# Kernel tuning notes

Hardware: AMD Instinct MI355X
Metric: run time of the kernel (lower is better)

The kernel has to match this reference:

```python
import jax, jax.numpy as jnp
import numpy as np

SELECTED_NUM = 4096
BN_EPS = 1e-5


def _conv1d(x, w, pad):
    # x: [B, C_in, L], w: [C_out, C_in, K]
    return jax.lax.conv_general_dilated(
        x, w, window_strides=(1,), padding=[(pad, pad)],
        dimension_numbers=('NCH', 'OIH', 'NCH'))


def _bn(x, g, b, m, v):
    # eval-mode BatchNorm1d over channel dim of [B, C, L]
    inv = g / jnp.sqrt(v + BN_EPS)
    return x * inv[None, :, None] + (b - m * inv)[None, :, None]


def setup_inputs() -> dict:
    key = jax.random.key(0)
    ks = jax.random.split(key, 16)
    B, N, CODE, NCLS = 4, 262144, 7, 3
    inp = {
        'box_preds': jax.random.normal(ks[0], (B, N, CODE), jnp.float32),
        'cls_preds': jax.random.normal(ks[1], (B, N, NCLS), jnp.float32),
        # conv_share: Conv1d(10,32,3) + BN(32) + ReLU + Conv1d(32,64,3) + BN(64) + ReLU
        'conv1_w': jax.random.normal(ks[2], (32, 10, 3), jnp.float32) * 0.1,
        'bn1_g': jax.random.uniform(ks[3], (32,), jnp.float32, 0.5, 1.5),
        'bn1_b': jax.random.normal(ks[4], (32,), jnp.float32) * 0.1,
        'bn1_m': jax.random.normal(ks[5], (32,), jnp.float32) * 0.1,
        'bn1_v': jax.random.uniform(ks[6], (32,), jnp.float32, 0.5, 1.5),
        'conv2_w': jax.random.normal(ks[7], (64, 32, 3), jnp.float32) * 0.1,
        'bn2_g': jax.random.uniform(ks[8], (64,), jnp.float32, 0.5, 1.5),
        'bn2_b': jax.random.normal(ks[9], (64,), jnp.float32) * 0.1,
        'bn2_m': jax.random.normal(ks[10], (64,), jnp.float32) * 0.1,
        'bn2_v': jax.random.uniform(ks[11], (64,), jnp.float32, 0.5, 1.5),
        # heads: Conv1d(64,5,1,bias=True), Conv1d(64,1,1,bias=True)
        'bin_w': jax.random.normal(ks[12], (5, 64, 1), jnp.float32) * 0.1,
        'bin_b': jnp.full((5,), -float(np.log((1 - 0.01) / 0.01)), jnp.float32),
        'res_w': jax.random.normal(ks[13], (1, 64, 1), jnp.float32) * 0.001,
        'res_b': jnp.zeros((1,), jnp.float32),
    }
    return inp


def reference(box_preds, cls_preds, conv1_w, bn1_g, bn1_b, bn1_m, bn1_v,
              conv2_w, bn2_g, bn2_b, bn2_m, bn2_v, bin_w, bin_b, res_w, res_b):
    # ---- proposal_layer: per-batch sigmoid(max-cls-score) topk + gather ----
    score = jax.nn.sigmoid(jnp.max(cls_preds, axis=-1))          # [B, N]
    _, sel = jax.lax.top_k(score, SELECTED_NUM)                  # [B, K]
    box_sel = jnp.take_along_axis(box_preds, sel[:, :, None], axis=1)  # [B, K, 7]
    cls_sel = jnp.take_along_axis(cls_preds, sel[:, :, None], axis=1)  # [B, K, 3]

    # ---- conv_share + heads over channel-first layout [B, 10, K] ----
    x = jnp.concatenate([box_sel, cls_sel], axis=-1).transpose(0, 2, 1)  # [B, 10, K]
    x = jax.nn.relu(_bn(_conv1d(x, conv1_w, 1), bn1_g, bn1_b, bn1_m, bn1_v))
    x = jax.nn.relu(_bn(_conv1d(x, conv2_w, 1), bn2_g, bn2_b, bn2_m, bn2_v))  # [B, 64, K]

    iou_bin = _conv1d(x, bin_w, 0) + bin_b[None, :, None]        # [B, 5, K]
    iou_res = _conv1d(x, res_w, 0) + res_b[None, :, None]        # [B, 1, K]

    iou_preds_bin = iou_bin.transpose(0, 2, 1)                   # [B, K, 5]
    iou_preds_residual = iou_res.transpose(0, 2, 1)              # [B, K, 1]
    return iou_preds_bin, iou_preds_residual, box_sel, cls_sel
```

## Files before the change

### kernel.cpp

```cpp
#include <hip/hip_runtime.h>
#include <stdint.h>

#define NPTS 262144
#define NB 4
#define KSEL 4096
#define CAP 8192
#define SLICE_LEN 1024
#define CBLK 128
#define HBLK 64

#define OFF_BITS  0ULL
#define OFF_H8P   (4ULL*NPTS*NB)
#define OFF_H12   (OFF_H8P + 4ULL*256*HBLK*NB)
#define OFF_CTRL  (OFF_H12 + 4ULL*4096*NB)
#define OFF_GRANK (OFF_CTRL + 1024ULL)
#define OFF_CAND  (OFF_GRANK + 4ULL*CAP*NB)
#define WS_NEEDED (OFF_CAND + 8ULL*CAP*NB)

#define OBIN 0
#define ORES (NB*KSEL*5)
#define OBOX (ORES + NB*KSEL)
#define OCLS (OBOX + NB*KSEL*7)


__device__ __forceinline__ uint32_t key_of(float mx) {
    uint32_t b = __float_as_uint(mx);
    uint32_t mask = ((int32_t)b >> 31) | 0x80000000u;
    return b ^ mask;
}

__device__ __forceinline__ void suffix_scan_256(volatile uint32_t* part, int tid) {
    #pragma unroll
    for (int off = 1; off < 256; off <<= 1) {
        uint32_t v = part[tid] + ((tid + off < 256) ? part[tid + off] : 0u);
        __syncthreads();
        part[tid] = v;
        __syncthreads();
    }
}

__global__ __launch_bounds__(256) void k_score_hist(
    const float* __restrict__ cls, uint32_t* __restrict__ bits, uint32_t* __restrict__ h8p,
    uint32_t* __restrict__ h12, uint32_t* __restrict__ grank, uint32_t* __restrict__ ctrl)
{
    __shared__ uint32_t lh[8][256];
    for (int i = threadIdx.x; i < 2048; i += 256) ((uint32_t*)lh)[i] = 0;
    __syncthreads();
    int b = blockIdx.y, bx = blockIdx.x;
    int sub = threadIdx.x >> 5;
    for (int it = 0; it < 4; ++it) {
        int chunk = bx * 1024 + it * 256 + threadIdx.x;
        const float4* p = (const float4*)(cls + ((size_t)b * NPTS + (size_t)chunk * 4) * 3);
        float4 v0 = p[0], v1 = p[1], v2 = p[2];
        uint4 o;
        o.x = key_of(fmaxf(fmaxf(v0.x, v0.y), v0.z));
        o.y = key_of(fmaxf(fmaxf(v0.w, v1.x), v1.y));
        o.z = key_of(fmaxf(fmaxf(v1.z, v1.w), v2.x));
        o.w = key_of(fmaxf(fmaxf(v2.y, v2.z), v2.w));
        ((uint4*)(bits + (size_t)b * NPTS))[chunk] = o;
        atomicAdd(&lh[sub][o.x >> 24], 1u);
        atomicAdd(&lh[sub][o.y >> 24], 1u);
        atomicAdd(&lh[sub][o.z >> 24], 1u);
        atomicAdd(&lh[sub][o.w >> 24], 1u);
    }
    if (bx == 1) {
        uint4* z = (uint4*)(h12 + (size_t)b * 4096);
        #pragma unroll
        for (int i = 0; i < 4; ++i) z[threadIdx.x + i * 256] = make_uint4(0u, 0u, 0u, 0u);
    } else if (bx == 2) {
        uint4* zg = (uint4*)(grank + (size_t)b * CAP);
        #pragma unroll
        for (int i = 0; i < 8; ++i) zg[threadIdx.x + i * 256] = make_uint4(0u, 0u, 0u, 0u);
    } else if (bx == 3 && threadIdx.x == 0) {
        ctrl[b * 16 + 3] = 0u;
    }
    __syncthreads();
    uint32_t c = 0;
    #pragma unroll
    for (int s = 0; s < 8; ++s) c += lh[s][threadIdx.x];
    h8p[((size_t)b * HBLK + bx) * 256 + threadIdx.x] = c;
}

__global__ __launch_bounds__(256) void k_hist12(
    const uint32_t* __restrict__ bits, const uint32_t* __restrict__ h8p,
    uint32_t* __restrict__ ctrl, uint32_t* __restrict__ h12)
{
    __shared__ uint32_t lh[4096];
    __shared__ uint32_t part[257];
    __shared__ uint32_t P8s;
    int b = blockIdx.y, bx = blockIdx.x;
    int tid = threadIdx.x;
    for (int i = tid; i < 4096; i += 256) lh[i] = 0;
    uint32_t sum = 0;
    const uint32_t* hp = h8p + (size_t)b * HBLK * 256 + tid;
    #pragma unroll 8
    for (int blk = 0; blk < HBLK; ++blk) sum += hp[blk * 256];
    part[tid] = sum;
    if (tid == 0) part[256] = 0u;
    __syncthreads();
    suffix_scan_256(part, tid);
    {
        uint32_t si = part[tid], sn = part[tid + 1];
        if (si >= (uint32_t)KSEL && sn < (uint32_t)KSEL) {
            P8s = (uint32_t)tid;
            if (bx == 0) { ctrl[b * 16 + 0] = (uint32_t)tid; ctrl[b * 16 + 1] = sn; }
        }
    }
    __syncthreads();
    const uint32_t P8 = P8s;
    for (int it = 0; it < 4; ++it) {
        int chunk = bx * 1024 + it * 256 + tid;
        uint4 v = ((const uint4*)(bits + (size_t)b * NPTS))[chunk];
        if ((v.x >> 24) == P8) atomicAdd(&lh[(v.x >> 12) & 0xFFFu], 1u);
        if ((v.y >> 24) == P8) atomicAdd(&lh[(v.y >> 12) & 0xFFFu], 1u);
        if ((v.z >> 24) == P8) atomicAdd(&lh[(v.z >> 12) & 0xFFFu], 1u);
        if ((v.w >> 24) == P8) atomicAdd(&lh[(v.w >> 12) & 0xFFFu], 1u);
    }
    __syncthreads();
    for (int i = tid; i < 4096; i += 256) {
        uint32_t c = lh[i];
        if (c) atomicAdd(&h12[(size_t)b * 4096 + i], c);
    }
}

__global__ __launch_bounds__(256) void k_compact(
    const uint32_t* __restrict__ bits, const uint32_t* __restrict__ h12,
    uint32_t* __restrict__ ctrl, uint64_t* __restrict__ cand)
{
    __shared__ uint32_t bins[4096];
    __shared__ uint32_t part[257];
    __shared__ uint32_t segS, Ts;
    __shared__ uint32_t wbase[4];
    int b = blockIdx.y, bx = blockIdx.x;
    int tid = threadIdx.x;
    const uint4* src = (const uint4*)(h12 + (size_t)b * 4096);
    for (int i = tid; i < 1024; i += 256) ((uint4*)bins)[i] = src[i];
    __syncthreads();
    {
        uint32_t s = 0;
        int base2 = tid * 16;
        #pragma unroll
        for (int j = 0; j < 16; ++j) s += bins[base2 + j];
        part[tid] = s;
        if (tid == 0) part[256] = 0u;
    }
    __syncthreads();
    const uint32_t K = (uint32_t)KSEL - ctrl[b * 16 + 1];
    suffix_scan_256(part, tid);
    {
        uint32_t si = part[tid], sn = part[tid + 1];
        if (si >= K && sn < K) segS = (uint32_t)tid;
    }
    __syncthreads();
    if (tid < 16) {
        uint32_t seg = segS;
        uint32_t above = part[seg + 1];
        uint32_t cnt = above;
        for (int j = 15; j >= tid; --j) cnt += bins[seg * 16 + j];
        uint32_t cntn = cnt - bins[seg * 16 + tid];
        if (cnt >= K && cntn < K) {
            Ts = (ctrl[b * 16 + 0] << 12) | (seg * 16 + (uint32_t)tid);
        }
    }
    __syncthreads();
    const uint32_t T = Ts;
    const int lane = tid & 63, wave = tid >> 6;
    const uint64_t lmask = (1ull << lane) - 1ull;

    int chunk0 = bx * 512 + tid;
    const uint4* sb = (const uint4*)(bits + (size_t)b * NPTS);
    uint4 v0 = sb[chunk0];
    uint4 v1 = sb[chunk0 + 256];
    uint32_t ks[8] = {v0.x, v0.y, v0.z, v0.w, v1.x, v1.y, v1.z, v1.w};
    bool sel[8];
    #pragma unroll
    for (int i = 0; i < 8; ++i) sel[i] = (ks[i] >> 12) >= T;

    uint32_t wsum = 0;
    #pragma unroll
    for (int i = 0; i < 8; ++i) wsum += (uint32_t)__popcll(__ballot(sel[i]));
    if (lane == 0) wbase[wave] = wsum;
    __syncthreads();
    if (tid == 0) {
        uint32_t c0 = wbase[0], c1 = wbase[1], c2 = wbase[2], c3 = wbase[3];
        uint32_t tot = c0 + c1 + c2 + c3;
        uint32_t base = tot ? atomicAdd(&ctrl[b * 16 + 3], tot) : 0u;
        wbase[0] = base;
        wbase[1] = base + c0;
        wbase[2] = base + c0 + c1;
        wbase[3] = base + c0 + c1 + c2;
    }
    __syncthreads();
    uint32_t off = wbase[wave];
    #pragma unroll
    for (int i = 0; i < 8; ++i) {
        uint64_t m = __ballot(sel[i]);
        if (sel[i]) {
            uint32_t pos = off + (uint32_t)__popcll(m & lmask);
            uint32_t n = (uint32_t)(chunk0 + (i < 4 ? 0 : 256)) * 4 + (uint32_t)(i & 3);
            if (pos < CAP)
                cand[(size_t)b * CAP + pos] = ((uint64_t)(~ks[i]) << 32) | (uint64_t)n;
        }
        off += (uint32_t)__popcll(m);
    }
}

__global__ __launch_bounds__(256) void k_rank1(
    const uint64_t* __restrict__ cand, const uint32_t* __restrict__ ctrl,
    uint32_t* __restrict__ grank)
{
    __shared__ uint64_t keys[SLICE_LEN];
    int b = blockIdx.z;
    uint32_t C = ctrl[b * 16 + 3];
    if (C > CAP) C = CAP;
    uint32_t ig0 = blockIdx.x * 1024;
    uint32_t sk0 = blockIdx.y * SLICE_LEN;
    if (ig0 >= C || sk0 >= C) return;
    uint32_t nk = C - sk0; if (nk > SLICE_LEN) nk = SLICE_LEN;
    const uint64_t* cb = cand + (size_t)b * CAP;
    for (uint32_t i = threadIdx.x; i < nk; i += 256) keys[i] = cb[sk0 + i];
    __syncthreads();
    uint64_t me[4];
    uint32_t idx[4], r[4] = {0u, 0u, 0u, 0u};
    #pragma unroll
    for (int q = 0; q < 4; ++q) {
        idx[q] = ig0 + (uint32_t)q * 256 + threadIdx.x;
        me[q] = (idx[q] < C) ? cb[idx[q]] : ~0ull;
    }
    #pragma unroll 8
    for (uint32_t i = 0; i < nk; ++i) {
        uint64_t k = keys[i];
        r[0] += (k < me[0]) ? 1u : 0u;
        r[1] += (k < me[1]) ? 1u : 0u;
        r[2] += (k < me[2]) ? 1u : 0u;
        r[3] += (k < me[3]) ? 1u : 0u;
    }
    #pragma unroll
    for (int q = 0; q < 4; ++q)
        if (idx[q] < C) atomicAdd(&grank[b * CAP + idx[q]], r[q]);
}

__global__ __launch_bounds__(256) void k_rank2(
    const uint64_t* __restrict__ cand, const uint32_t* __restrict__ ctrl,
    const uint32_t* __restrict__ grank,
    const float* __restrict__ box, const float* __restrict__ cls, float* __restrict__ out)
{
    int b = blockIdx.y;
    uint32_t C = ctrl[b * 16 + 3];
    if (C > CAP) C = CAP;
    uint32_t item = blockIdx.x * 256 + threadIdx.x;
    if (blockIdx.x * 256 >= C) return;
    if (item >= C) return;
    uint64_t me = cand[(size_t)b * CAP + item];
    uint32_t rank = grank[b * CAP + item];
    if (rank < KSEL) {
        uint32_t n = (uint32_t)me;
        const float* bp = box + ((size_t)b * NPTS + n) * 7;
        float* ob = out + OBOX + ((size_t)b * KSEL + rank) * 7;
        #pragma unroll
        for (int c = 0; c < 7; ++c) ob[c] = bp[c];
        const float* cp = cls + ((size_t)b * NPTS + n) * 3;
        float* oc = out + OCLS + ((size_t)b * KSEL + rank) * 3;
        #pragma unroll
        for (int c = 0; c < 3; ++c) oc[c] = cp[c];
    }
}

__global__ __launch_bounds__(256) void k_conv(
    const float* __restrict__ c1w, const float* __restrict__ g1v, const float* __restrict__ b1v,
    const float* __restrict__ m1v, const float* __restrict__ v1v,
    const float* __restrict__ c2w, const float* __restrict__ g2v, const float* __restrict__ b2v,
    const float* __restrict__ m2v, const float* __restrict__ v2v,
    const float* __restrict__ binw, const float* __restrict__ binb,
    const float* __restrict__ resw, const float* __restrict__ resb,
    float* __restrict__ out)
{
    __shared__ __align__(16) float w1s[960];
    __shared__ __align__(16) float b1s[32];
    __shared__ __align__(16) float w2s[6144];
    __shared__ __align__(16) float b2s[64];
    __shared__ __align__(16) float hws[6][64];
    __shared__ __align__(16) float xin[10][80];
    __shared__ __align__(16) float x1s[32][68];
    __shared__ __align__(16) float x2t[64][68];

    int tid = threadIdx.x;
    int b = blockIdx.y;
    int tile0 = blockIdx.x * 64;
    const float* boxsel = out + OBOX + (size_t)b * KSEL * 7;
    const float* clssel = out + OCLS + (size_t)b * KSEL * 3;

    for (int t = tid; t < 960; t += 256) {
        int c = t / 30, r = t - c * 30, i = r / 3, tap = r - i * 3;
        float inv = g1v[c] * rsqrtf(v1v[c] + 1e-5f);
        w1s[(i * 3 + tap) * 32 + c] = c1w[t] * inv;
    }
    if (tid < 32) {
        float inv = g1v[tid] * rsqrtf(v1v[tid] + 1e-5f);
        b1s[tid] = b1v[tid] - m1v[tid] * inv;
    }
    for (int t = tid; t < 6144; t += 256) {
        int o = t / 96, r = t - o * 96, i = r / 3, tap = r - i * 3;
        float inv = g2v[o] * rsqrtf(v2v[o] + 1e-5f);
        w2s[(i * 3 + tap) * 64 + o] = c2w[t] * inv;
    }
    if (tid >= 64 && tid < 128) {
        int o = tid - 64;
        float inv = g2v[o] * rsqrtf(v2v[o] + 1e-5f);
        b2s[o] = b2v[o] - m2v[o] * inv;
    }
    for (int t = tid; t < 384; t += 256)
        ((float*)hws)[t] = (t < 320) ? binw[t] : resw[t - 320];

    for (int u = tid; u < 680; u += 256) {
        int c = u / 68, k2 = u - c * 68;
        int g = tile0 + k2 - 2;
        float val = 0.f;
        if (g >= 0 && g < KSEL) val = (c < 7) ? boxsel[g * 7 + c] : clssel[g * 3 + (c - 7)];
        xin[c][k2] = val;
    }
    __syncthreads();

    {
        int c = tid & 31, kg = tid >> 5;
        int k0 = kg * 9;
        int nk = 66 - k0; if (nk > 9) nk = 9;
        float a[9];
        #pragma unroll
        for (int kk = 0; kk < 9; ++kk) a[kk] = b1s[c];
        #pragma unroll 2
        for (int i = 0; i < 10; ++i) {
            float xv[11];
            #pragma unroll
            for (int j = 0; j < 11; ++j) xv[j] = xin[i][k0 + j];
            #pragma unroll
            for (int tap = 0; tap < 3; ++tap) {
                float w = w1s[(i * 3 + tap) * 32 + c];
                #pragma unroll
                for (int kk = 0; kk < 9; ++kk) a[kk] = fmaf(w, xv[kk + tap], a[kk]);
            }
        }
        for (int kk = 0; kk < nk; ++kk) {
            int k = k0 + kk, gp = tile0 + k - 1;
            x1s[c][k] = (gp >= 0 && gp < KSEL) ? fmaxf(a[kk], 0.f) : 0.f;
        }
    }
    __syncthreads();

    {
        int o = tid & 63, pg = tid >> 6;
        int p0 = pg * 16;
        float acc[16];
        float bz = b2s[o];
        #pragma unroll
        for (int kk = 0; kk < 16; ++kk) acc[kk] = bz;
        #pragma unroll 4
        for (int i = 0; i < 32; ++i) {
            float4 xq[5];
            const float4* xr = (const float4*)&x1s[i][p0];
            #pragma unroll
            for (int q = 0; q < 5; ++q) xq[q] = xr[q];
            const float* xf = (const float*)xq;
            float w0 = w2s[(i * 3 + 0) * 64 + o];
            float w1 = w2s[(i * 3 + 1) * 64 + o];
            float w2 = w2s[(i * 3 + 2) * 64 + o];
            #pragma unroll
            for (int kk = 0; kk < 16; ++kk) {
                float t0 = fmaf(w0, xf[kk], acc[kk]);
                t0 = fmaf(w1, xf[kk + 1], t0);
                acc[kk] = fmaf(w2, xf[kk + 2], t0);
            }
        }
        #pragma unroll
        for (int kk = 0; kk < 16; ++kk)
            x2t[p0 + kk][o] = fmaxf(acc[kk], 0.f);
    }
    __syncthreads();

    {
        int p = tid & 63, g = tid >> 6;
        const float4* xr = (const float4*)&x2t[p][0];
        const float4* hw4 = (const float4*)hws;
        size_t gpos = (size_t)b * KSEL + (size_t)(tile0 + p);
        if (g < 2) {
            int j0 = g * 2, j1 = j0 + 1;
            float s0 = 0.f, s1 = 0.f;
            #pragma unroll
            for (int q = 0; q < 16; ++q) {
                float4 xv = xr[q];
                float4 wa = hw4[j0 * 16 + q];
                float4 wb = hw4[j1 * 16 + q];
                s0 = fmaf(xv.x, wa.x, s0); s0 = fmaf(xv.y, wa.y, s0);
                s0 = fmaf(xv.z, wa.z, s0); s0 = fmaf(xv.w, wa.w, s0);
                s1 = fmaf(xv.x, wb.x, s1); s1 = fmaf(xv.y, wb.y, s1);
                s1 = fmaf(xv.z, wb.z, s1); s1 = fmaf(xv.w, wb.w, s1);
            }
            out[OBIN + gpos * 5 + j0] = s0 + binb[j0];
            out[OBIN + gpos * 5 + j1] = s1 + binb[j1];
        } else {
            int j = (g == 2) ? 4 : 5;
            float s = 0.f;
            #pragma unroll
            for (int q = 0; q < 16; ++q) {
                float4 xv = xr[q];
                float4 wa = hw4[j * 16 + q];
                s = fmaf(xv.x, wa.x, s); s = fmaf(xv.y, wa.y, s);
                s = fmaf(xv.z, wa.z, s); s = fmaf(xv.w, wa.w, s);
            }
            if (g == 2) out[OBIN + gpos * 5 + 4] = s + binb[4];
            else        out[ORES + gpos]         = s + resb[0];
        }
    }
}

extern "C" void kernel_launch(void* const* d_in, const int* in_sizes, int n_in,
                              void* d_out, int out_size, void* d_ws, size_t ws_size,
                              hipStream_t stream)
{
    const float* box  = (const float*)d_in[0];
    const float* cls  = (const float*)d_in[1];
    const float* c1w  = (const float*)d_in[2];
    const float* g1   = (const float*)d_in[3];
    const float* b1   = (const float*)d_in[4];
    const float* m1   = (const float*)d_in[5];
    const float* v1   = (const float*)d_in[6];
    const float* c2w  = (const float*)d_in[7];
    const float* g2   = (const float*)d_in[8];
    const float* b2   = (const float*)d_in[9];
    const float* m2   = (const float*)d_in[10];
    const float* v2   = (const float*)d_in[11];
    const float* binw = (const float*)d_in[12];
    const float* binb = (const float*)d_in[13];
    const float* resw = (const float*)d_in[14];
    const float* resb = (const float*)d_in[15];
    float* out = (float*)d_out;
    char* ws = (char*)d_ws;
    if (ws_size < WS_NEEDED) return;

    uint32_t* bits  = (uint32_t*)(ws + OFF_BITS);
    uint32_t* h8p   = (uint32_t*)(ws + OFF_H8P);
    uint32_t* h12   = (uint32_t*)(ws + OFF_H12);
    uint32_t* ctrl  = (uint32_t*)(ws + OFF_CTRL);
    uint32_t* grank = (uint32_t*)(ws + OFF_GRANK);
    uint64_t* cand  = (uint64_t*)(ws + OFF_CAND);

    k_score_hist<<<dim3(HBLK, NB), 256, 0, stream>>>(cls, bits, h8p, h12, grank, ctrl);
    k_hist12<<<dim3(HBLK, NB), 256, 0, stream>>>(bits, h8p, ctrl, h12);
    k_compact<<<dim3(CBLK, NB), 256, 0, stream>>>(bits, h12, ctrl, cand);
    k_rank1<<<dim3(CAP / 1024, CAP / 1024, NB), 256, 0, stream>>>(cand, ctrl, grank);
    k_rank2<<<dim3(CAP / 256, NB), 256, 0, stream>>>(cand, ctrl, grank, box, cls, out);
    k_conv<<<dim3(64, NB), 256, 0, stream>>>(c1w, g1, b1, m1, v1, c2w, g2, b2, m2, v2,
                                             binw, binb, resw, resb, out);
}
```

Measured before the change: 75.63 us.

## Replace two-pass radix select with single 16-bit histogram and last-block threshold

The 8-bit then 12-bit histogram passes are replaced by one 16-bit key histogram built while the keys are computed. A fixed window of bins near the expected top scores is counted in shared memory, and everything else goes straight to global atomics. The last block to finish, detected with an atomic counter, scans the histogram and writes the threshold, so the second pass over the keys and the threshold search in k_compact both go away. The cost is coarser threshold bins, hence more candidates, and possible global-atomic contention when scores fall outside the window.

```diff
diff --git a/kernel.cpp b/kernel.cpp
--- a/kernel.cpp
+++ b/kernel.cpp
@@ -6,13 +6,13 @@
 #define KSEL 4096
 #define CAP 8192
 #define SLICE_LEN 1024
-#define CBLK 128
-#define HBLK 64
+#define KBLK 256
+#define WIN_LO 0xB800u
+#define WIN_N  0x1000u
 
 #define OFF_BITS  0ULL
-#define OFF_H8P   (4ULL*NPTS*NB)
-#define OFF_H12   (OFF_H8P + 4ULL*256*HBLK*NB)
-#define OFF_CTRL  (OFF_H12 + 4ULL*4096*NB)
+#define OFF_H16   (4ULL*NPTS*NB)
+#define OFF_CTRL  (OFF_H16 + 4ULL*65536*NB)
 #define OFF_GRANK (OFF_CTRL + 1024ULL)
 #define OFF_CAND  (OFF_GRANK + 4ULL*CAP*NB)
 #define WS_NEEDED (OFF_CAND + 8ULL*CAP*NB)
@@ -39,152 +39,121 @@
     }
 }
 
-__global__ __launch_bounds__(256) void k_score_hist(
-    const float* __restrict__ cls, uint32_t* __restrict__ bits, uint32_t* __restrict__ h8p,
-    uint32_t* __restrict__ h12, uint32_t* __restrict__ grank, uint32_t* __restrict__ ctrl)
-{
-    __shared__ uint32_t lh[8][256];
-    for (int i = threadIdx.x; i < 2048; i += 256) ((uint32_t*)lh)[i] = 0;
-    __syncthreads();
-    int b = blockIdx.y, bx = blockIdx.x;
-    int sub = threadIdx.x >> 5;
-    for (int it = 0; it < 4; ++it) {
-        int chunk = bx * 1024 + it * 256 + threadIdx.x;
-        const float4* p = (const float4*)(cls + ((size_t)b * NPTS + (size_t)chunk * 4) * 3);
-        float4 v0 = p[0], v1 = p[1], v2 = p[2];
-        uint4 o;
-        o.x = key_of(fmaxf(fmaxf(v0.x, v0.y), v0.z));
-        o.y = key_of(fmaxf(fmaxf(v0.w, v1.x), v1.y));
-        o.z = key_of(fmaxf(fmaxf(v1.z, v1.w), v2.x));
-        o.w = key_of(fmaxf(fmaxf(v2.y, v2.z), v2.w));
-        ((uint4*)(bits + (size_t)b * NPTS))[chunk] = o;
-        atomicAdd(&lh[sub][o.x >> 24], 1u);
-        atomicAdd(&lh[sub][o.y >> 24], 1u);
-        atomicAdd(&lh[sub][o.z >> 24], 1u);
-        atomicAdd(&lh[sub][o.w >> 24], 1u);
-    }
-    if (bx == 1) {
-        uint4* z = (uint4*)(h12 + (size_t)b * 4096);
-        #pragma unroll
-        for (int i = 0; i < 4; ++i) z[threadIdx.x + i * 256] = make_uint4(0u, 0u, 0u, 0u);
-    } else if (bx == 2) {
-        uint4* zg = (uint4*)(grank + (size_t)b * CAP);
-        #pragma unroll
-        for (int i = 0; i < 8; ++i) zg[threadIdx.x + i * 256] = make_uint4(0u, 0u, 0u, 0u);
-    } else if (bx == 3 && threadIdx.x == 0) {
-        ctrl[b * 16 + 3] = 0u;
-    }
-    __syncthreads();
-    uint32_t c = 0;
-    #pragma unroll
-    for (int s = 0; s < 8; ++s) c += lh[s][threadIdx.x];
-    h8p[((size_t)b * HBLK + bx) * 256 + threadIdx.x] = c;
-}
-
-__global__ __launch_bounds__(256) void k_hist12(
-    const uint32_t* __restrict__ bits, const uint32_t* __restrict__ h8p,
-    uint32_t* __restrict__ ctrl, uint32_t* __restrict__ h12)
-{
-    __shared__ uint32_t lh[4096];
+__global__ __launch_bounds__(256) void k_init(
+    uint4* __restrict__ h16v, uint4* __restrict__ grankv, uint32_t* __restrict__ ctrl)
+{
+    int bx = blockIdx.x, tid = threadIdx.x;
+    uint4 z = make_uint4(0u, 0u, 0u, 0u);
+    if (bx < 32) {
+        int i = bx * 2048 + tid;
+        #pragma unroll
+        for (int k = 0; k < 8; ++k) h16v[i + k * 256] = z;
+    } else {
+        int i = (bx - 32) * 1024 + tid;
+        #pragma unroll
+        for (int k = 0; k < 4; ++k) grankv[i + k * 256] = z;
+        if (bx == 32 && tid < 64) ctrl[tid] = 0u;
+    }
+}
+
+__global__ __launch_bounds__(256) void k_keys(
+    const float* __restrict__ cls, uint32_t* __restrict__ bits,
+    uint32_t* __restrict__ h16, uint32_t* __restrict__ ctrl)
+{
+    __shared__ uint32_t lh[WIN_N];
     __shared__ uint32_t part[257];
-    __shared__ uint32_t P8s;
-    int b = blockIdx.y, bx = blockIdx.x;
-    int tid = threadIdx.x;
-    for (int i = tid; i < 4096; i += 256) lh[i] = 0;
-    uint32_t sum = 0;
-    const uint32_t* hp = h8p + (size_t)b * HBLK * 256 + tid;
-    #pragma unroll 8
-    for (int blk = 0; blk < HBLK; ++blk) sum += hp[blk * 256];
-    part[tid] = sum;
+    __shared__ uint32_t segS, aboveS;
+    __shared__ int amLastS;
+    int b = blockIdx.y, bx = blockIdx.x, tid = threadIdx.x;
+    for (int i = tid; i < (int)WIN_N; i += 256) lh[i] = 0;
+    __syncthreads();
+
+    int chunk = bx * 256 + tid;
+    const float4* p = (const float4*)(cls + ((size_t)b * NPTS + (size_t)chunk * 4) * 3);
+    float4 v0 = p[0], v1 = p[1], v2 = p[2];
+    uint4 o;
+    o.x = key_of(fmaxf(fmaxf(v0.x, v0.y), v0.z));
+    o.y = key_of(fmaxf(fmaxf(v0.w, v1.x), v1.y));
+    o.z = key_of(fmaxf(fmaxf(v1.z, v1.w), v2.x));
+    o.w = key_of(fmaxf(fmaxf(v2.y, v2.z), v2.w));
+    ((uint4*)(bits + (size_t)b * NPTS))[chunk] = o;
+    uint32_t ks[4] = {o.x, o.y, o.z, o.w};
+    uint32_t* h16b = h16 + (size_t)b * 65536;
+    #pragma unroll
+    for (int i = 0; i < 4; ++i) {
+        uint32_t hi = ks[i] >> 16;
+        uint32_t d = hi - WIN_LO;
+        if (d < WIN_N) atomicAdd(&lh[d], 1u);
+        else           atomicAdd(&h16b[hi], 1u);
+    }
+    __syncthreads();
+    for (int i = tid; i < (int)WIN_N; i += 256) {
+        uint32_t c = lh[i];
+        if (c) atomicAdd(&h16b[WIN_LO + i], c);
+    }
+    __syncthreads();
+    __threadfence();
+    if (tid == 0) {
+        uint32_t r = atomicAdd(&ctrl[b * 16 + 15], 1u);
+        amLastS = (r == (uint32_t)(KBLK - 1));
+    }
+    __syncthreads();
+    if (!amLastS) return;
+
+    const uint4* h4 = (const uint4*)h16b;
+    uint32_t s = 0;
+    #pragma unroll 16
+    for (int q = 0; q < 64; ++q) {
+        uint4 v = h4[tid * 64 + q];
+        s += v.x + v.y + v.z + v.w;
+    }
+    part[tid] = s;
+    if (tid == 0) part[256] = 0u;
+    __syncthreads();
+    suffix_scan_256(part, tid);
+    if (part[tid] >= (uint32_t)KSEL && part[tid + 1] < (uint32_t)KSEL) segS = (uint32_t)tid;
+    __syncthreads();
+    if (tid == 0) aboveS = part[segS + 1];
+    __syncthreads();
+    uint32_t binv = h16b[segS * 256 + tid];
+    __syncthreads();
+    part[tid] = binv;
     if (tid == 0) part[256] = 0u;
     __syncthreads();
     suffix_scan_256(part, tid);
     {
-        uint32_t si = part[tid], sn = part[tid + 1];
-        if (si >= (uint32_t)KSEL && sn < (uint32_t)KSEL) {
-            P8s = (uint32_t)tid;
-            if (bx == 0) { ctrl[b * 16 + 0] = (uint32_t)tid; ctrl[b * 16 + 1] = sn; }
-        }
-    }
-    __syncthreads();
-    const uint32_t P8 = P8s;
-    for (int it = 0; it < 4; ++it) {
-        int chunk = bx * 1024 + it * 256 + tid;
-        uint4 v = ((const uint4*)(bits + (size_t)b * NPTS))[chunk];
-        if ((v.x >> 24) == P8) atomicAdd(&lh[(v.x >> 12) & 0xFFFu], 1u);
-        if ((v.y >> 24) == P8) atomicAdd(&lh[(v.y >> 12) & 0xFFFu], 1u);
-        if ((v.z >> 24) == P8) atomicAdd(&lh[(v.z >> 12) & 0xFFFu], 1u);
-        if ((v.w >> 24) == P8) atomicAdd(&lh[(v.w >> 12) & 0xFFFu], 1u);
-    }
-    __syncthreads();
-    for (int i = tid; i < 4096; i += 256) {
-        uint32_t c = lh[i];
-        if (c) atomicAdd(&h12[(size_t)b * 4096 + i], c);
+        uint32_t above = aboveS;
+        if (above + part[tid] >= (uint32_t)KSEL && above + part[tid + 1] < (uint32_t)KSEL)
+            ctrl[b * 16 + 2] = segS * 256 + (uint32_t)tid;
     }
 }
 
 __global__ __launch_bounds__(256) void k_compact(
-    const uint32_t* __restrict__ bits, const uint32_t* __restrict__ h12,
-    uint32_t* __restrict__ ctrl, uint64_t* __restrict__ cand)
-{
-    __shared__ uint32_t bins[4096];
-    __shared__ uint32_t part[257];
-    __shared__ uint32_t segS, Ts;
+    const uint32_t* __restrict__ bits, const uint32_t* __restrict__ ctrl,
+    uint64_t* __restrict__ cand)
+{
     __shared__ uint32_t wbase[4];
-    int b = blockIdx.y, bx = blockIdx.x;
-    int tid = threadIdx.x;
-    const uint4* src = (const uint4*)(h12 + (size_t)b * 4096);
-    for (int i = tid; i < 1024; i += 256) ((uint4*)bins)[i] = src[i];
-    __syncthreads();
-    {
-        uint32_t s = 0;
-        int base2 = tid * 16;
-        #pragma unroll
-        for (int j = 0; j < 16; ++j) s += bins[base2 + j];
-        part[tid] = s;
-        if (tid == 0) part[256] = 0u;
-    }
-    __syncthreads();
-    const uint32_t K = (uint32_t)KSEL - ctrl[b * 16 + 1];
-    suffix_scan_256(part, tid);
-    {
-        uint32_t si = part[tid], sn = part[tid + 1];
-        if (si >= K && sn < K) segS = (uint32_t)tid;
-    }
-    __syncthreads();
-    if (tid < 16) {
-        uint32_t seg = segS;
-        uint32_t above = part[seg + 1];
-        uint32_t cnt = above;
-        for (int j = 15; j >= tid; --j) cnt += bins[seg * 16 + j];
-        uint32_t cntn = cnt - bins[seg * 16 + tid];
-        if (cnt >= K && cntn < K) {
-            Ts = (ctrl[b * 16 + 0] << 12) | (seg * 16 + (uint32_t)tid);
-        }
-    }
-    __syncthreads();
-    const uint32_t T = Ts;
+    int b = blockIdx.y, tid = threadIdx.x;
+    uint32_t T = ctrl[b * 16 + 2];
     const int lane = tid & 63, wave = tid >> 6;
     const uint64_t lmask = (1ull << lane) - 1ull;
 
-    int chunk0 = bx * 512 + tid;
-    const uint4* sb = (const uint4*)(bits + (size_t)b * NPTS);
-    uint4 v0 = sb[chunk0];
-    uint4 v1 = sb[chunk0 + 256];
-    uint32_t ks[8] = {v0.x, v0.y, v0.z, v0.w, v1.x, v1.y, v1.z, v1.w};
-    bool sel[8];
-    #pragma unroll
-    for (int i = 0; i < 8; ++i) sel[i] = (ks[i] >> 12) >= T;
+    int chunk = blockIdx.x * 256 + tid;
+    uint4 v = ((const uint4*)(bits + (size_t)b * NPTS))[chunk];
+    uint32_t ks[4] = {v.x, v.y, v.z, v.w};
+    bool sel[4];
+    #pragma unroll
+    for (int i = 0; i < 4; ++i) sel[i] = (ks[i] >> 16) >= T;
 
     uint32_t wsum = 0;
     #pragma unroll
-    for (int i = 0; i < 8; ++i) wsum += (uint32_t)__popcll(__ballot(sel[i]));
+    for (int i = 0; i < 4; ++i) wsum += (uint32_t)__popcll(__ballot(sel[i]));
     if (lane == 0) wbase[wave] = wsum;
     __syncthreads();
     if (tid == 0) {
         uint32_t c0 = wbase[0], c1 = wbase[1], c2 = wbase[2], c3 = wbase[3];
         uint32_t tot = c0 + c1 + c2 + c3;
-        uint32_t base = tot ? atomicAdd(&ctrl[b * 16 + 3], tot) : 0u;
+        uint32_t base = tot ? atomicAdd((uint32_t*)&ctrl[b * 16 + 3], tot) : 0u;
         wbase[0] = base;
         wbase[1] = base + c0;
         wbase[2] = base + c0 + c1;
@@ -193,13 +162,13 @@
     __syncthreads();
     uint32_t off = wbase[wave];
     #pragma unroll
-    for (int i = 0; i < 8; ++i) {
+    for (int i = 0; i < 4; ++i) {
         uint64_t m = __ballot(sel[i]);
         if (sel[i]) {
             uint32_t pos = off + (uint32_t)__popcll(m & lmask);
-            uint32_t n = (uint32_t)(chunk0 + (i < 4 ? 0 : 256)) * 4 + (uint32_t)(i & 3);
             if (pos < CAP)
-                cand[(size_t)b * CAP + pos] = ((uint64_t)(~ks[i]) << 32) | (uint64_t)n;
+                cand[(size_t)b * CAP + pos] =
+                    ((uint64_t)(~ks[i]) << 32) | (uint64_t)((uint32_t)chunk * 4 + i);
         }
         off += (uint32_t)__popcll(m);
     }
@@ -438,15 +407,14 @@
     if (ws_size < WS_NEEDED) return;
 
     uint32_t* bits  = (uint32_t*)(ws + OFF_BITS);
-    uint32_t* h8p   = (uint32_t*)(ws + OFF_H8P);
-    uint32_t* h12   = (uint32_t*)(ws + OFF_H12);
+    uint32_t* h16   = (uint32_t*)(ws + OFF_H16);
     uint32_t* ctrl  = (uint32_t*)(ws + OFF_CTRL);
     uint32_t* grank = (uint32_t*)(ws + OFF_GRANK);
     uint64_t* cand  = (uint64_t*)(ws + OFF_CAND);
 
-    k_score_hist<<<dim3(HBLK, NB), 256, 0, stream>>>(cls, bits, h8p, h12, grank, ctrl);
-    k_hist12<<<dim3(HBLK, NB), 256, 0, stream>>>(bits, h8p, ctrl, h12);
-    k_compact<<<dim3(CBLK, NB), 256, 0, stream>>>(bits, h12, ctrl, cand);
+    k_init<<<40, 256, 0, stream>>>((uint4*)h16, (uint4*)grank, ctrl);
+    k_keys<<<dim3(KBLK, NB), 256, 0, stream>>>(cls, bits, h16, ctrl);
+    k_compact<<<dim3(256, NB), 256, 0, stream>>>(bits, ctrl, cand);
     k_rank1<<<dim3(CAP / 1024, CAP / 1024, NB), 256, 0, stream>>>(cand, ctrl, grank);
     k_rank2<<<dim3(CAP / 256, NB), 256, 0, stream>>>(cand, ctrl, grank, box, cls, out);
     k_conv<<<dim3(64, NB), 256, 0, stream>>>(c1w, g1, b1, m1, v1, c2w, g2, b2, m2, v2,
```

Measured after the change: 176.7 us. 2.34x slower.

## Fuse rank gather into rank kernel via last-block counter; halve conv tiles

Applied to the files above, without the earlier changes.

Merges k_rank2 into k_rank1: each item-group block increments a per-group counter in ctrl after adding its partial ranks, and the last slice block to finish does the gather of box/cls rows into the output. This removes one kernel launch. The conv kernel's tile shrinks from 64 to 32 points, doubling its grid to 128 blocks per batch and simplifying the head stage to one output per thread. The score histogram also moves to 16 sub-histograms to cut shared atomic contention. The fused gather relies on threadfence plus an atomic counter for correctness, and the smaller conv tile recomputes more halo and reloads weights per block.

```diff
diff --git a/kernel.cpp b/kernel.cpp
--- a/kernel.cpp
+++ b/kernel.cpp
@@ -43,11 +43,11 @@
     const float* __restrict__ cls, uint32_t* __restrict__ bits, uint32_t* __restrict__ h8p,
     uint32_t* __restrict__ h12, uint32_t* __restrict__ grank, uint32_t* __restrict__ ctrl)
 {
-    __shared__ uint32_t lh[8][256];
-    for (int i = threadIdx.x; i < 2048; i += 256) ((uint32_t*)lh)[i] = 0;
+    __shared__ uint32_t lh[16][256];
+    for (int i = threadIdx.x; i < 4096; i += 256) ((uint32_t*)lh)[i] = 0;
     __syncthreads();
     int b = blockIdx.y, bx = blockIdx.x;
-    int sub = threadIdx.x >> 5;
+    int sub = threadIdx.x >> 4;
     for (int it = 0; it < 4; ++it) {
         int chunk = bx * 1024 + it * 256 + threadIdx.x;
         const float4* p = (const float4*)(cls + ((size_t)b * NPTS + (size_t)chunk * 4) * 3);
@@ -71,13 +71,13 @@
         uint4* zg = (uint4*)(grank + (size_t)b * CAP);
         #pragma unroll
         for (int i = 0; i < 8; ++i) zg[threadIdx.x + i * 256] = make_uint4(0u, 0u, 0u, 0u);
-    } else if (bx == 3 && threadIdx.x == 0) {
-        ctrl[b * 16 + 3] = 0u;
+    } else if (bx == 3 && threadIdx.x < 9) {
+        ctrl[b * 16 + 3 + threadIdx.x] = 0u;
     }
     __syncthreads();
     uint32_t c = 0;
     #pragma unroll
-    for (int s = 0; s < 8; ++s) c += lh[s][threadIdx.x];
+    for (int s = 0; s < 16; ++s) c += lh[s][threadIdx.x];
     h8p[((size_t)b * HBLK + bx) * 256 + threadIdx.x] = c;
 }
 
@@ -158,9 +158,8 @@
         uint32_t cnt = above;
         for (int j = 15; j >= tid; --j) cnt += bins[seg * 16 + j];
         uint32_t cntn = cnt - bins[seg * 16 + tid];
-        if (cnt >= K && cntn < K) {
+        if (cnt >= K && cntn < K)
             Ts = (ctrl[b * 16 + 0] << 12) | (seg * 16 + (uint32_t)tid);
-        }
     }
     __syncthreads();
     const uint32_t T = Ts;
@@ -205,26 +204,30 @@
     }
 }
 
-__global__ __launch_bounds__(256) void k_rank1(
-    const uint64_t* __restrict__ cand, const uint32_t* __restrict__ ctrl,
-    uint32_t* __restrict__ grank)
+__global__ __launch_bounds__(256) void k_rank(
+    const uint64_t* __restrict__ cand, uint32_t* __restrict__ ctrl,
+    uint32_t* __restrict__ grank,
+    const float* __restrict__ box, const float* __restrict__ cls, float* __restrict__ out)
 {
     __shared__ uint64_t keys[SLICE_LEN];
-    int b = blockIdx.z;
+    __shared__ int lastS;
+    int b = blockIdx.z, tid = threadIdx.x;
     uint32_t C = ctrl[b * 16 + 3];
     if (C > CAP) C = CAP;
-    uint32_t ig0 = blockIdx.x * 1024;
+    uint32_t ig = blockIdx.x;
+    uint32_t ig0 = ig * 1024;
     uint32_t sk0 = blockIdx.y * SLICE_LEN;
     if (ig0 >= C || sk0 >= C) return;
+    uint32_t Sact = (C + SLICE_LEN - 1) / SLICE_LEN;
     uint32_t nk = C - sk0; if (nk > SLICE_LEN) nk = SLICE_LEN;
     const uint64_t* cb = cand + (size_t)b * CAP;
-    for (uint32_t i = threadIdx.x; i < nk; i += 256) keys[i] = cb[sk0 + i];
+    for (uint32_t i = tid; i < nk; i += 256) keys[i] = cb[sk0 + i];
     __syncthreads();
     uint64_t me[4];
     uint32_t idx[4], r[4] = {0u, 0u, 0u, 0u};
     #pragma unroll
     for (int q = 0; q < 4; ++q) {
-        idx[q] = ig0 + (uint32_t)q * 256 + threadIdx.x;
+        idx[q] = ig0 + (uint32_t)q * 256 + tid;
         me[q] = (idx[q] < C) ? cb[idx[q]] : ~0ull;
     }
     #pragma unroll 8
@@ -238,31 +241,31 @@
     #pragma unroll
     for (int q = 0; q < 4; ++q)
         if (idx[q] < C) atomicAdd(&grank[b * CAP + idx[q]], r[q]);
-}
-
-__global__ __launch_bounds__(256) void k_rank2(
-    const uint64_t* __restrict__ cand, const uint32_t* __restrict__ ctrl,
-    const uint32_t* __restrict__ grank,
-    const float* __restrict__ box, const float* __restrict__ cls, float* __restrict__ out)
-{
-    int b = blockIdx.y;
-    uint32_t C = ctrl[b * 16 + 3];
-    if (C > CAP) C = CAP;
-    uint32_t item = blockIdx.x * 256 + threadIdx.x;
-    if (blockIdx.x * 256 >= C) return;
-    if (item >= C) return;
-    uint64_t me = cand[(size_t)b * CAP + item];
-    uint32_t rank = grank[b * CAP + item];
-    if (rank < KSEL) {
-        uint32_t n = (uint32_t)me;
-        const float* bp = box + ((size_t)b * NPTS + n) * 7;
-        float* ob = out + OBOX + ((size_t)b * KSEL + rank) * 7;
-        #pragma unroll
-        for (int c = 0; c < 7; ++c) ob[c] = bp[c];
-        const float* cp = cls + ((size_t)b * NPTS + n) * 3;
-        float* oc = out + OCLS + ((size_t)b * KSEL + rank) * 3;
-        #pragma unroll
-        for (int c = 0; c < 3; ++c) oc[c] = cp[c];
+    __syncthreads();
+    __threadfence();
+    if (tid == 0) {
+        uint32_t old = atomicAdd(&ctrl[b * 16 + 4 + ig], 1u);
+        lastS = (old == Sact - 1);
+    }
+    __syncthreads();
+    if (!lastS) return;
+    #pragma unroll
+    for (int q = 0; q < 4; ++q) {
+        uint32_t it = ig0 + (uint32_t)q * 256 + tid;
+        if (it < C) {
+            uint32_t rank = grank[b * CAP + it];
+            if (rank < KSEL) {
+                uint32_t n = (uint32_t)cb[it];
+                const float* bp = box + ((size_t)b * NPTS + n) * 7;
+                float* ob = out + OBOX + ((size_t)b * KSEL + rank) * 7;
+                #pragma unroll
+                for (int c = 0; c < 7; ++c) ob[c] = bp[c];
+                const float* cp = cls + ((size_t)b * NPTS + n) * 3;
+                float* oc = out + OCLS + ((size_t)b * KSEL + rank) * 3;
+                #pragma unroll
+                for (int c = 0; c < 3; ++c) oc[c] = cp[c];
+            }
+        }
     }
 }
 
@@ -280,13 +283,13 @@
     __shared__ __align__(16) float w2s[6144];
     __shared__ __align__(16) float b2s[64];
     __shared__ __align__(16) float hws[6][64];
-    __shared__ __align__(16) float xin[10][80];
-    __shared__ __align__(16) float x1s[32][68];
-    __shared__ __align__(16) float x2t[64][68];
+    __shared__ __align__(16) float xin[10][40];
+    __shared__ __align__(16) float x1s[32][36];
+    __shared__ __align__(16) float x2t[32][68];
 
     int tid = threadIdx.x;
     int b = blockIdx.y;
-    int tile0 = blockIdx.x * 64;
+    int tile0 = blockIdx.x * 32;
     const float* boxsel = out + OBOX + (size_t)b * KSEL * 7;
     const float* clssel = out + OCLS + (size_t)b * KSEL * 3;
 
@@ -312,8 +315,8 @@
     for (int t = tid; t < 384; t += 256)
         ((float*)hws)[t] = (t < 320) ? binw[t] : resw[t - 320];
 
-    for (int u = tid; u < 680; u += 256) {
-        int c = u / 68, k2 = u - c * 68;
+    for (int u = tid; u < 360; u += 256) {
+        int c = u / 36, k2 = u - c * 36;
         int g = tile0 + k2 - 2;
         float val = 0.f;
         if (g >= 0 && g < KSEL) val = (c < 7) ? boxsel[g * 7 + c] : clssel[g * 3 + (c - 7)];
@@ -323,92 +326,78 @@
 
     {
         int c = tid & 31, kg = tid >> 5;
-        int k0 = kg * 9;
-        int nk = 66 - k0; if (nk > 9) nk = 9;
-        float a[9];
-        #pragma unroll
-        for (int kk = 0; kk < 9; ++kk) a[kk] = b1s[c];
-        #pragma unroll 2
-        for (int i = 0; i < 10; ++i) {
-            float xv[11];
-            #pragma unroll
-            for (int j = 0; j < 11; ++j) xv[j] = xin[i][k0 + j];
-            #pragma unroll
-            for (int tap = 0; tap < 3; ++tap) {
-                float w = w1s[(i * 3 + tap) * 32 + c];
+        int k0 = kg * 5;
+        int nk = 34 - k0; if (nk > 5) nk = 5; if (nk < 0) nk = 0;
+        float a[5];
+        #pragma unroll
+        for (int kk = 0; kk < 5; ++kk) a[kk] = b1s[c];
+        if (nk > 0) {
+            #pragma unroll 2
+            for (int i = 0; i < 10; ++i) {
+                float xv[7];
                 #pragma unroll
-                for (int kk = 0; kk < 9; ++kk) a[kk] = fmaf(w, xv[kk + tap], a[kk]);
+                for (int j = 0; j < 7; ++j) xv[j] = xin[i][k0 + j];
+                #pragma unroll
+                for (int tap = 0; tap < 3; ++tap) {
+                    float w = w1s[(i * 3 + tap) * 32 + c];
+                    #pragma unroll
+                    for (int kk = 0; kk < 5; ++kk) a[kk] = fmaf(w, xv[kk + tap], a[kk]);
+                }
             }
-        }
-        for (int kk = 0; kk < nk; ++kk) {
-            int k = k0 + kk, gp = tile0 + k - 1;
-            x1s[c][k] = (gp >= 0 && gp < KSEL) ? fmaxf(a[kk], 0.f) : 0.f;
+            for (int kk = 0; kk < nk; ++kk) {
+                int k = k0 + kk, gp = tile0 + k - 1;
+                x1s[c][k] = (gp >= 0 && gp < KSEL) ? fmaxf(a[kk], 0.f) : 0.f;
+            }
         }
     }
     __syncthreads();
 
     {
         int o = tid & 63, pg = tid >> 6;
-        int p0 = pg * 16;
-        float acc[16];
+        int p0 = pg * 8;
+        float acc[8];
         float bz = b2s[o];
         #pragma unroll
-        for (int kk = 0; kk < 16; ++kk) acc[kk] = bz;
+        for (int kk = 0; kk < 8; ++kk) acc[kk] = bz;
         #pragma unroll 4
         for (int i = 0; i < 32; ++i) {
-            float4 xq[5];
+            float4 xq[3];
             const float4* xr = (const float4*)&x1s[i][p0];
             #pragma unroll
-            for (int q = 0; q < 5; ++q) xq[q] = xr[q];
+            for (int q = 0; q < 3; ++q) xq[q] = xr[q];
             const float* xf = (const float*)xq;
             float w0 = w2s[(i * 3 + 0) * 64 + o];
             float w1 = w2s[(i * 3 + 1) * 64 + o];
             float w2 = w2s[(i * 3 + 2) * 64 + o];
             #pragma unroll
-            for (int kk = 0; kk < 16; ++kk) {
+            for (int kk = 0; kk < 8; ++kk) {
                 float t0 = fmaf(w0, xf[kk], acc[kk]);
                 t0 = fmaf(w1, xf[kk + 1], t0);
                 acc[kk] = fmaf(w2, xf[kk + 2], t0);
             }
         }
         #pragma unroll
-        for (int kk = 0; kk < 16; ++kk)
+        for (int kk = 0; kk < 8; ++kk)
             x2t[p0 + kk][o] = fmaxf(acc[kk], 0.f);
     }
     __syncthreads();
 
     {
-        int p = tid & 63, g = tid >> 6;
-        const float4* xr = (const float4*)&x2t[p][0];
-        const float4* hw4 = (const float4*)hws;
-        size_t gpos = (size_t)b * KSEL + (size_t)(tile0 + p);
-        if (g < 2) {
-            int j0 = g * 2, j1 = j0 + 1;
-            float s0 = 0.f, s1 = 0.f;
-            #pragma unroll
-            for (int q = 0; q < 16; ++q) {
-                float4 xv = xr[q];
-                float4 wa = hw4[j0 * 16 + q];
-                float4 wb = hw4[j1 * 16 + q];
-                s0 = fmaf(xv.x, wa.x, s0); s0 = fmaf(xv.y, wa.y, s0);
-                s0 = fmaf(xv.z, wa.z, s0); s0 = fmaf(xv.w, wa.w, s0);
-                s1 = fmaf(xv.x, wb.x, s1); s1 = fmaf(xv.y, wb.y, s1);
-                s1 = fmaf(xv.z, wb.z, s1); s1 = fmaf(xv.w, wb.w, s1);
-            }
-            out[OBIN + gpos * 5 + j0] = s0 + binb[j0];
-            out[OBIN + gpos * 5 + j1] = s1 + binb[j1];
-        } else {
-            int j = (g == 2) ? 4 : 5;
+        int p = tid & 31, g = tid >> 5;
+        if (g < 6) {
+            const float4* xr = (const float4*)&x2t[p][0];
+            const float4* hw4 = (const float4*)hws;
+            size_t gpos = (size_t)b * KSEL + (size_t)(tile0 + p);
             float s = 0.f;
             #pragma unroll
             for (int q = 0; q < 16; ++q) {
                 float4 xv = xr[q];
-                float4 wa = hw4[j * 16 + q];
+                float4 wa = hw4[g * 16 + q];
                 s = fmaf(xv.x, wa.x, s); s = fmaf(xv.y, wa.y, s);
                 s = fmaf(xv.z, wa.z, s); s = fmaf(xv.w, wa.w, s);
             }
-            if (g == 2) out[OBIN + gpos * 5 + 4] = s + binb[4];
-            else        out[ORES + gpos]         = s + resb[0];
+            if (g < 5) out[OBIN + gpos * 5 + g] = s + binb[g];
+            else       out[ORES + gpos]         = s + resb[0];
         }
     }
 }
@@ -447,8 +436,7 @@
     k_score_hist<<<dim3(HBLK, NB), 256, 0, stream>>>(cls, bits, h8p, h12, grank, ctrl);
     k_hist12<<<dim3(HBLK, NB), 256, 0, stream>>>(bits, h8p, ctrl, h12);
     k_compact<<<dim3(CBLK, NB), 256, 0, stream>>>(bits, h12, ctrl, cand);
-    k_rank1<<<dim3(CAP / 1024, CAP / 1024, NB), 256, 0, stream>>>(cand, ctrl, grank);
-    k_rank2<<<dim3(CAP / 256, NB), 256, 0, stream>>>(cand, ctrl, grank, box, cls, out);
-    k_conv<<<dim3(64, NB), 256, 0, stream>>>(c1w, g1, b1, m1, v1, c2w, g2, b2, m2, v2,
-                                             binw, binb, resw, resb, out);
-}
+    k_rank<<<dim3(CAP / 1024, CAP / 1024, NB), 256, 0, stream>>>(cand, ctrl, grank, box, cls, out);
+    k_conv<<<dim3(128, NB), 256, 0, stream>>>(c1w, g1, b1, m1, v1, c2w, g2, b2, m2, v2,
+                                              binw, binb, resw, resb, out);
+}
```

New measurement: 84.97 us. 12.4% more time.
